# Performance work log

Measured on AMD Instinct MI355X. Metric: run time of the kernel, lower is better.

Reference implementation:

```python
import jax, jax.numpy as jnp
import numpy as np

NB_SITES = 16
K = 32            # nb_intervals
H = 512           # hidden_dim
EMB = 8           # embedding_dim
OUT = 3 * K + 3   # widths K + heights K + derivs K+1 + center_x + center_y
D = EMB * (NB_SITES - 1)
MIN_BIN = 1e-3
MIN_DER = 1e-3
B = 4096


def invsymlu(x):
    # inverse symmetric linear unit: x+1 for x>=0, 1/(1-x) for x<0
    return jnp.where(x >= 0, x + 1.0, 1.0 / (1.0 - x))


def freq_embed(x):
    # (...,) -> (..., EMB): 4 sin + 4 cos frequencies
    div = jnp.exp(jnp.arange(0, EMB, 2, dtype=jnp.float32) * (-jnp.log(100.0) / EMB))
    xe = x[..., None] * div
    return jnp.concatenate([jnp.sin(xe), jnp.cos(xe)], axis=-1)


def layernorm(x, s, b, eps=1e-6):
    m = jnp.mean(x, axis=-1, keepdims=True)
    v = jnp.var(x, axis=-1, keepdims=True)
    return (x - m) * jax.lax.rsqrt(v + eps) * s + b


def rqs_forward(inputs, uw, uh, ud, cx, cy):
    # inputs: (B,S); uw/uh: (B,S,K); ud: (B,S,K+1); cx/cy: (B,S)
    widths = MIN_BIN + invsymlu(uw)
    heights = MIN_BIN + invsymlu(uh)
    derivatives = MIN_DER + invsymlu(ud)

    pad = [(0, 0)] * (widths.ndim - 1) + [(1, 0)]
    cumwidths = jnp.pad(jnp.cumsum(widths, axis=-1), pad)
    cumwidths = cumwidths - cumwidths[..., -1:] / 2 + cx[..., None]
    cumheights = jnp.pad(jnp.cumsum(heights, axis=-1), pad)
    cumheights = cumheights - cumheights[..., -1:] / 2 + cy[..., None]

    left = inputs < cumwidths[..., 0]
    right = inputs >= cumwidths[..., -1]
    outputs = jnp.where(left, cumheights[..., 0] - (cumwidths[..., 0] - inputs) * derivatives[..., 0], 0.0)
    outputs = jnp.where(right, (inputs - cumwidths[..., -1]) * derivatives[..., -1] + cumheights[..., -1], outputs)
    logabsdet = jnp.where(left, jnp.log(derivatives[..., 0]), 0.0)
    logabsdet = jnp.where(right, jnp.log(derivatives[..., -1]), logabsdet)
    inside = ~(left | right)

    xs = jnp.where(inside, inputs, cx)
    # searchsorted via broadcast compare over K+1 knots
    bin_idx = (jnp.sum((xs[..., None] >= cumwidths), axis=-1) - 1)[..., None]

    take = lambda a: jnp.take_along_axis(a, bin_idx, axis=-1)[..., 0]
    icw = take(cumwidths)
    ibw = take(widths)
    ich = take(cumheights)
    delta = heights / widths
    idl = take(delta)
    ider = take(derivatives)
    iderp = take(derivatives[..., 1:])
    ih = take(heights)

    theta = (xs - icw) / ibw
    tomt = theta * (1 - theta)
    num = ih * (idl * theta ** 2 + ider * tomt)
    den = idl + (ider + iderp - 2 * idl) * tomt
    outputs = jnp.where(inside, ich + num / den, outputs)
    dnum = idl ** 2 * (iderp * theta ** 2 + 2 * idl * tomt + ider * (1 - theta) ** 2)
    logabsdet = jnp.where(inside, jnp.log(dnum) - 2 * jnp.log(den), logabsdet)
    return outputs, logabsdet


def setup_inputs() -> dict:
    ks = jax.random.split(jax.random.key(0), 8)
    S1 = NB_SITES - 1
    x = jax.random.normal(ks[0], (B, NB_SITES), jnp.float32)
    bias0 = jax.random.normal(ks[1], (OUT,), jnp.float32) * 0.1
    W0 = jax.random.normal(ks[2], (S1, D, H), jnp.float32) * (2.0 / D) ** 0.5
    W1 = jax.random.normal(ks[3], (S1, H, H), jnp.float32) * (2.0 / H) ** 0.5
    W2 = jax.random.normal(ks[4], (S1, H, H), jnp.float32) * (2.0 / H) ** 0.5
    Wf = jax.random.normal(ks[5], (S1, H, OUT), jnp.float32) * (2.0 / H) ** 0.5
    zH = jnp.zeros((S1, H), jnp.float32)
    oH = jnp.ones((S1, H), jnp.float32)
    return dict(x=x, bias0=bias0,
                W0=W0, b0=zH, ln0s=oH, ln0b=zH,
                W1=W1, b1=zH, ln1s=oH, ln1b=zH,
                W2=W2, b2=zH, ln2s=oH, ln2b=zH,
                Wf=Wf, bf=jnp.zeros((S1, OUT), jnp.float32))


def reference(x, bias0, W0, b0, ln0s, ln0b, W1, b1, ln1s, ln1b, W2, b2, ln2s, ln2b, Wf, bf):
    Bn = x.shape[0]
    S1 = NB_SITES - 1
    # embeddings of sites 0..S-2, flattened site-major: (B, D)
    e = freq_embed(x[:, :S1]).reshape(Bn, D)
    # causal per-site mask: site s (1..S-1) sees first EMB*s features
    site = jnp.arange(1, NB_SITES)
    mask = (jnp.arange(D)[None, :] < EMB * site[:, None]).astype(x.dtype)  # (S-1, D)
    Wm = W0 * mask[:, :, None]

    h = jnp.einsum('bd,sdh->bsh', e, Wm) + b0
    h = layernorm(jax.nn.gelu(h), ln0s, ln0b)
    y = jnp.einsum('bsh,shk->bsk', h, W1) + b1 + h   # residual
    y = layernorm(jax.nn.gelu(y), ln1s, ln1b)
    z = jnp.einsum('bsh,shk->bsk', y, W2) + b2 + y   # residual
    z = layernorm(jax.nn.gelu(z), ln2s, ln2b)
    p = jnp.einsum('bsh,sho->bso', z, Wf) + bf        # (B, S-1, OUT)

    p0 = jnp.broadcast_to(bias0, (Bn, 1, OUT))        # site 0: BiasOnlyNet
    params = jnp.concatenate([p0, p], axis=1)         # (B, S, OUT)

    uw = params[..., :K]
    uh = params[..., K:2 * K]
    ud = params[..., 2 * K:3 * K + 1]
    cx = params[..., 3 * K + 1]
    cy = params[..., 3 * K + 2]
    out, lad = rqs_forward(x, uw, uh, ud, cx, cy)
    return out, lad.sum(-1)
```

## Files before the change

kernel.cpp:

```cpp
#include <hip/hip_runtime.h>
#include <hip/hip_bf16.h>
#include <cstdint>
#include <cstddef>

typedef _Float16 f16;
typedef __attribute__((ext_vector_type(8))) _Float16 f16x8;
typedef __attribute__((ext_vector_type(4))) float f32x4;

#define DI __device__ __forceinline__

constexpr int BATCH  = 4096;
constexpr int S1     = 15;
constexpr int DPAD   = 128;
constexpr int H      = 512;
constexpr int OUTC   = 99;
constexpr int OUTPAD = 112;

DI float gelu_tanh(float x) {
  float t = 1.5957691216057308f * (x + 0.044715f * x * x * x);
  return x / (1.f + __expf(-t));
}

DI void gload16(const void* g, void* l) {
  __builtin_amdgcn_global_load_lds(
      (const __attribute__((address_space(1))) void*)g,
      (__attribute__((address_space(3))) void*)l, 16, 0, 0);
}

__global__ void embed_kernel(const float* __restrict__ x, f16* __restrict__ e) {
  const int b = blockIdx.x, d = threadIdx.x;
  float v = 0.f;
  if (d < 120) {
    const float divs[4] = {1.f, 0.31622776601683794f, 0.1f, 0.03162277660168379f};
    int site = d >> 3, j = d & 7;
    float arg = x[b * 16 + site] * divs[j & 3];
    v = (j < 4) ? sinf(arg) : cosf(arg);
  }
  e[b * DPAD + d] = (f16)v;
}

__global__ __launch_bounds__(256) void transpose_conv_kernel(
    const float* __restrict__ src, f16* __restrict__ dsth, f16* __restrict__ dstl,
    int K, int N, int Kpad, int Npad, int maskMul) {
  __shared__ float tile[32][33];
  const int s  = blockIdx.z;
  const int kb = blockIdx.x * 32, nb = blockIdx.y * 32;
  const int tx = threadIdx.x & 31, ty = threadIdx.x >> 5;
  for (int i = ty; i < 32; i += 8) {
    int k = kb + i, n = nb + tx;
    tile[i][tx] = (k < K && n < N) ? src[((size_t)s * K + k) * N + n] : 0.f;
  }
  __syncthreads();
  const int klim = maskMul ? maskMul * (s + 1) : 0x7FFFFFFF;
  for (int i = ty; i < 32; i += 8) {
    int n = nb + i, k = kb + tx;
    if (n < Npad && k < Kpad) {
      float v = (k < klim) ? tile[tx][i] : 0.f;
      size_t o = ((size_t)s * Npad + n) * Kpad + k;
      f16 h = (f16)v;
      dsth[o] = h;
      dstl[o] = (f16)(v - (float)h);
    }
  }
}

template<bool RES>
__global__ __launch_bounds__(512) void gemm_ln_kernel(
    const f16* __restrict__ A, const f16* __restrict__ Wh, const f16* __restrict__ Wl,
    const float* __restrict__ bias, const float* __restrict__ lns,
    const float* __restrict__ lnb, f16* __restrict__ out,
    int M, int Kd, int strideAS) {
  constexpr int BM = 64, BN = 512, BK = 64;
  constexpr int WM = 32, WN = 128, FM = 2, FN = 8;
  extern __shared__ f16 smem[];
  f16* const Aev = smem;
  f16* const Aod = smem + BM * BK;
  f16* const B0  = smem + 2 * BM * BK;
  f16* const B1  = B0 + BN * BK;

  const int n    = gridDim.x;
  const int b    = blockIdx.x;
  const int w    = (b & 7) * (n >> 3) + (b >> 3);
  const int srel = w >> 6;
  const int m0   = (w & 63) * BM;

  const f16* ap  = A  + (size_t)srel * strideAS + (size_t)m0 * Kd;
  const f16* wph = Wh + (size_t)srel * BN * Kd;
  const f16* wpl = Wl + (size_t)srel * BN * Kd;
  const int tid = threadIdx.x, wbase = tid & ~63;
  const int wave = tid >> 6, lane = tid & 63;
  const int wr = wave >> 2, wc = wave & 3;
  const int laneRow = lane & 15;
  const int hi      = lane >> 4;

  const int rA  = tid >> 3;
  const int cg8 = (((tid & 7) ^ (rA & 7)) << 3);
  const uint32_t offA = (uint32_t)rA * (uint32_t)Kd + cg8;
  uint32_t offB[8];
#pragma unroll
  for (int j = 0; j < 8; ++j)
    offB[j] = (uint32_t)(j * 64 + rA) * (uint32_t)Kd + cg8;

  auto stageB = [&](const f16* __restrict__ gbase, uint32_t koff, f16* lds) {
#pragma unroll
    for (int j = 0; j < 8; ++j)
      gload16(gbase + offB[j] + koff, lds + ((j * 512 + wbase) << 3));
  };
  auto stageA = [&](uint32_t koff, f16* lds) {
    gload16(ap + offA + koff, lds + (wbase << 3));
  };

  f32x4 acc[FM][FN] = {};
  auto mma = [&](const f16* __restrict__ Ab, const f16* __restrict__ Bb) {
#pragma unroll
    for (int kk = 0; kk < BK / 32; ++kk) {
      const int cc = kk * 4 + hi;
      f16x8 a[FM];
#pragma unroll
      for (int mi = 0; mi < FM; ++mi) {
        const int row = wr * WM + mi * 16 + laneRow;
        a[mi] = *reinterpret_cast<const f16x8*>(&Ab[row * BK + ((cc ^ (row & 7)) << 3)]);
      }
#pragma unroll
      for (int ni = 0; ni < FN; ++ni) {
        const int row = wc * WN + ni * 16 + laneRow;
        f16x8 bv = *reinterpret_cast<const f16x8*>(&Bb[row * BK + ((cc ^ (row & 7)) << 3)]);
#pragma unroll
        for (int mi = 0; mi < FM; ++mi)
          acc[mi][ni] = __builtin_amdgcn_mfma_f32_16x16x32_f16(a[mi], bv, acc[mi][ni], 0, 0, 0);
      }
    }
  };

  stageA(0, Aev);
  stageB(wph, 0, B0);
  const int NT = Kd / BK;
  for (int t = 0; t < NT; t += 2) {
    __syncthreads();
    stageB(wpl, (uint32_t)t * BK, B1);
    mma(Aev, B0);
    __syncthreads();
    stageA((uint32_t)(t + 1) * BK, Aod);
    stageB(wph, (uint32_t)(t + 1) * BK, B0);
    mma(Aev, B1);
    __syncthreads();
    stageB(wpl, (uint32_t)(t + 1) * BK, B1);
    mma(Aod, B0);
    __syncthreads();
    if (t + 2 < NT) {
      stageA((uint32_t)(t + 2) * BK, Aev);
      stageB(wph, (uint32_t)(t + 2) * BK, B0);
    }
    mma(Aod, B1);
  }

  const int rbase = hi * 4;
  float bv[FN], sv[FN], bb[FN];
#pragma unroll
  for (int ni = 0; ni < FN; ++ni) {
    const int gn = wc * WN + ni * 16 + laneRow;
    bv[ni] = bias[srel * H + gn];
    sv[ni] = lns[srel * H + gn];
    bb[ni] = lnb[srel * H + gn];
  }
  float lsum[FM][4], lsq[FM][4];
#pragma unroll
  for (int mi = 0; mi < FM; ++mi)
#pragma unroll
    for (int r = 0; r < 4; ++r) { lsum[mi][r] = 0.f; lsq[mi][r] = 0.f; }
#pragma unroll
  for (int mi = 0; mi < FM; ++mi)
#pragma unroll
    for (int r = 0; r < 4; ++r) {
      const int row = wr * WM + mi * 16 + rbase + r;
#pragma unroll
      for (int ni = 0; ni < FN; ++ni) {
        const int gn = wc * WN + ni * 16 + laneRow;
        float y = acc[mi][ni][r] + bv[ni];
        if constexpr (RES)
          y += (float)A[(size_t)srel * strideAS + (size_t)(m0 + row) * Kd + gn];
        float g = gelu_tanh(y);
        acc[mi][ni][r] = g;
        lsum[mi][r] += g;
        lsq[mi][r]  += g * g;
      }
    }
#pragma unroll
  for (int o = 1; o < 16; o <<= 1)
#pragma unroll
    for (int mi = 0; mi < FM; ++mi)
#pragma unroll
      for (int r = 0; r < 4; ++r) {
        lsum[mi][r] += __shfl_xor(lsum[mi][r], o, 64);
        lsq[mi][r]  += __shfl_xor(lsq[mi][r], o, 64);
      }
  __syncthreads();
  float* red = reinterpret_cast<float*>(smem);
  if (laneRow == 0) {
#pragma unroll
    for (int mi = 0; mi < FM; ++mi)
#pragma unroll
      for (int r = 0; r < 4; ++r) {
        const int row = wr * WM + mi * 16 + rbase + r;
        red[(row * 4 + wc) * 2 + 0] = lsum[mi][r];
        red[(row * 4 + wc) * 2 + 1] = lsq[mi][r];
      }
  }
  __syncthreads();
#pragma unroll
  for (int mi = 0; mi < FM; ++mi)
#pragma unroll
    for (int r = 0; r < 4; ++r) {
      const int row = wr * WM + mi * 16 + rbase + r;
      float sum = 0.f, sq = 0.f;
#pragma unroll
      for (int w4 = 0; w4 < 4; ++w4) {
        sum += red[(row * 4 + w4) * 2 + 0];
        sq  += red[(row * 4 + w4) * 2 + 1];
      }
      const float mean = sum * (1.f / 512.f);
      const float var  = sq * (1.f / 512.f) - mean * mean;
      const float rstd = 1.f / sqrtf(var + 1e-6f);
#pragma unroll
      for (int ni = 0; ni < FN; ++ni) {
        const int gn = wc * WN + ni * 16 + laneRow;
        float z = (acc[mi][ni][r] - mean) * rstd * sv[ni] + bb[ni];
        out[((size_t)srel * M + m0 + row) * H + gn] = (f16)z;
      }
    }
}

__global__ __launch_bounds__(512) void gemm_out_kernel(
    const f16* __restrict__ A, const f16* __restrict__ Wh, const f16* __restrict__ Wl,
    const float* __restrict__ bias, float* __restrict__ out,
    int M, int Kd, int strideAS) {
  constexpr int BM = 128, BN = 112, BK = 64;
  constexpr int CPR = BK / 8, SWZ = CPR - 1;
  constexpr int FN = 7;
  extern __shared__ f16 smem[];
  f16* As  = smem;
  f16* Bhs = As + BM * BK;
  f16* Bls = Bhs + BN * BK;

  const int s  = blockIdx.z;
  const int m0 = blockIdx.x * BM;
  const f16* ap  = A  + (size_t)s * strideAS + (size_t)m0 * Kd;
  const f16* wph = Wh + (size_t)s * BN * Kd;
  const f16* wpl = Wl + (size_t)s * BN * Kd;
  const int tid = threadIdx.x, wbase = tid & ~63;
  const int wave = tid >> 6, lane = tid & 63;
  const int wr = wave;
  f32x4 acc[FN] = {};
  const int laneRow = lane & 15;
  const int hi      = lane >> 4;

  for (int k0 = 0; k0 < Kd; k0 += BK) {
    __syncthreads();
#pragma unroll
    for (int base = 0; base < BM * CPR; base += 512) {
      const int idx = base + tid;
      const int r = idx / CPR, c = idx % CPR, cg = c ^ (r & SWZ);
      gload16(ap + (size_t)r * Kd + k0 + cg * 8, As + (size_t)(base + wbase) * 8);
    }
#pragma unroll
    for (int base = 0; base < BN * CPR; base += 512) {
      const int idx = base + tid;
      if (idx < BN * CPR) {
        const int r = idx / CPR, c = idx % CPR, cg = c ^ (r & SWZ);
        const size_t go = (size_t)r * Kd + k0 + cg * 8;
        gload16(wph + go, Bhs + (size_t)(base + wbase) * 8);
        gload16(wpl + go, Bls + (size_t)(base + wbase) * 8);
      }
    }
    __syncthreads();
#pragma unroll
    for (int kk = 0; kk < BK / 32; ++kk) {
      const int cc = kk * 4 + hi;
      const int rowA = wr * 16 + laneRow;
      f16x8 a = *reinterpret_cast<const f16x8*>(&As[rowA * BK + ((cc ^ (rowA & SWZ)) << 3)]);
#pragma unroll
      for (int ni = 0; ni < FN; ++ni) {
        const int row = ni * 16 + laneRow;
        const int off = row * BK + ((cc ^ (row & SWZ)) << 3);
        f16x8 bh = *reinterpret_cast<const f16x8*>(&Bhs[off]);
        f16x8 bl = *reinterpret_cast<const f16x8*>(&Bls[off]);
        acc[ni] = __builtin_amdgcn_mfma_f32_16x16x32_f16(a, bh, acc[ni], 0, 0, 0);
        acc[ni] = __builtin_amdgcn_mfma_f32_16x16x32_f16(a, bl, acc[ni], 0, 0, 0);
      }
    }
  }

  const int rbase = hi * 4;
#pragma unroll
  for (int ni = 0; ni < FN; ++ni)
#pragma unroll
    for (int r = 0; r < 4; ++r) {
      const int gm = m0 + wr * 16 + rbase + r;
      const int gn = ni * 16 + laneRow;
      if (gn < OUTC)
        out[((size_t)s * M + gm) * OUTC + gn] = acc[ni][r] + bias[s * OUTC + gn];
    }
}

DI float invsymlu(float u) { return u >= 0.f ? u + 1.f : 1.f / (1.f - u); }

__global__ __launch_bounds__(128) void spline_kernel(
    const float* __restrict__ x, const float* __restrict__ bias0,
    const float* __restrict__ p, float* __restrict__ out0, float* __restrict__ ladbuf) {
  __shared__ float prm[128 * 101];
  const int i  = blockIdx.x;
  const int b0 = blockIdx.y * 128;
  if (i == 0) {
    for (int idx = threadIdx.x; idx < 128 * OUTC; idx += 128)
      prm[(idx / OUTC) * 101 + idx % OUTC] = bias0[idx % OUTC];
  } else {
    const float* src = p + ((size_t)(i - 1) * BATCH + b0) * OUTC;
    for (int idx = threadIdx.x; idx < 128 * OUTC; idx += 128)
      prm[(idx / OUTC) * 101 + idx % OUTC] = src[idx];
  }
  __syncthreads();
  const float* P = &prm[threadIdx.x * 101];
  const int b = b0 + threadIdx.x;
  const float inp = x[b * 16 + i];

  float tw = 0.f, th = 0.f;
  for (int k = 0; k < 32; ++k) tw += 0.001f + invsymlu(P[k]);
  for (int k = 0; k < 32; ++k) th += 0.001f + invsymlu(P[32 + k]);
  const float cx = P[97], cy = P[98];
  const float w0 = cx - 0.5f * tw, wK = cx + 0.5f * tw;
  const float h0 = cy - 0.5f * th, hK = cy + 0.5f * th;
  const float d0 = 0.001f + invsymlu(P[64]);
  const float dK = 0.001f + invsymlu(P[96]);
  float outv, lad;
  if (inp < w0) {
    outv = h0 - (w0 - inp) * d0;
    lad  = logf(d0);
  } else if (inp >= wK) {
    outv = (inp - wK) * dK + hK;
    lad  = logf(dK);
  } else {
    float run = w0, icw = w0, ibw = 1.f;
    int bin = 0;
    for (int k = 0; k < 32; ++k) {
      float wk = 0.001f + invsymlu(P[k]);
      if (inp >= run) { bin = k; icw = run; ibw = wk; }
      run += wk;
    }
    float runh = h0;
    for (int k = 0; k < bin; ++k) runh += 0.001f + invsymlu(P[32 + k]);
    const float ih    = 0.001f + invsymlu(P[32 + bin]);
    const float ich   = runh;
    const float ider  = 0.001f + invsymlu(P[64 + bin]);
    const float iderp = 0.001f + invsymlu(P[64 + bin + 1]);
    const float idl   = ih / ibw;
    const float theta = (inp - icw) / ibw;
    const float omt   = 1.f - theta;
    const float tomt  = theta * omt;
    const float num   = ih * (idl * theta * theta + ider * tomt);
    const float den   = idl + (ider + iderp - 2.f * idl) * tomt;
    outv = ich + num / den;
    const float dnum = idl * idl * (iderp * theta * theta + 2.f * idl * tomt + ider * omt * omt);
    lad = logf(dnum) - 2.f * logf(den);
  }
  out0[b * 16 + i]   = outv;
  ladbuf[b * 16 + i] = lad;
}

__global__ void lad_reduce_kernel(const float* __restrict__ ladbuf, float* __restrict__ out1) {
  const int b = blockIdx.x * 256 + threadIdx.x;
  float s = 0.f;
#pragma unroll
  for (int i = 0; i < 16; ++i) s += ladbuf[b * 16 + i];
  out1[b] = s;
}

extern "C" void kernel_launch(void* const* d_in, const int* in_sizes, int n_in,
                              void* d_out, int out_size, void* d_ws, size_t ws_size,
                              hipStream_t stream) {
  const float* x     = (const float*)d_in[0];
  const float* bias0 = (const float*)d_in[1];
  const float* W0    = (const float*)d_in[2];
  const float* b0    = (const float*)d_in[3];
  const float* ln0s  = (const float*)d_in[4];
  const float* ln0b  = (const float*)d_in[5];
  const float* W1    = (const float*)d_in[6];
  const float* b1    = (const float*)d_in[7];
  const float* ln1s  = (const float*)d_in[8];
  const float* ln1b  = (const float*)d_in[9];
  const float* W2    = (const float*)d_in[10];
  const float* b2    = (const float*)d_in[11];
  const float* ln2s  = (const float*)d_in[12];
  const float* ln2b  = (const float*)d_in[13];
  const float* Wf    = (const float*)d_in[14];
  const float* bfb   = (const float*)d_in[15];
  float* out0 = (float*)d_out;
  float* out1 = out0 + BATCH * 16;

  const size_t fixedBytes =
      (size_t)BATCH * DPAD * 2 +
      2 * ((size_t)S1 * H * DPAD * 2) +
      4 * ((size_t)S1 * H * H * 2) +
      2 * ((size_t)S1 * OUTPAD * H * 2) +
      (size_t)S1 * BATCH * OUTC * 4 +
      (size_t)BATCH * 16 * 4 +
      64 * 256;
  const size_t perSiteP = 2 * ((size_t)BATCH * H * 2);
  int CH = 1;
  if (ws_size > fixedBytes) {
    size_t c = (ws_size - fixedBytes) / perSiteP;
    CH = (c >= (size_t)S1) ? S1 : (c < 1 ? 1 : (int)c);
  }
  const int nPasses = (S1 + CH - 1) / CH;
  const int baseSz  = S1 / nPasses;
  const int remSz   = S1 % nPasses;

  char* ws = (char*)d_ws;
  size_t off = 0;
  auto take = [&](size_t bytes) {
    char* q = ws + off;
    off += (bytes + 255) & ~(size_t)255;
    return q;
  };
  f16* e     = (f16*)take((size_t)BATCH * DPAD * 2);
  f16* W0Th  = (f16*)take((size_t)S1 * H * DPAD * 2);
  f16* W0Tl  = (f16*)take((size_t)S1 * H * DPAD * 2);
  f16* W1Th  = (f16*)take((size_t)S1 * H * H * 2);
  f16* W1Tl  = (f16*)take((size_t)S1 * H * H * 2);
  f16* W2Th  = (f16*)take((size_t)S1 * H * H * 2);
  f16* W2Tl  = (f16*)take((size_t)S1 * H * H * 2);
  f16* WfTh  = (f16*)take((size_t)S1 * OUTPAD * H * 2);
  f16* WfTl  = (f16*)take((size_t)S1 * OUTPAD * H * 2);
  f16* P1    = (f16*)take((size_t)CH * BATCH * H * 2);
  f16* P2    = (f16*)take((size_t)CH * BATCH * H * 2);
  float* pbuf = (float*)take((size_t)S1 * BATCH * OUTC * 4);
  float* ladb = (float*)take((size_t)BATCH * 16 * 4);

  embed_kernel<<<BATCH, 128, 0, stream>>>(x, e);
  transpose_conv_kernel<<<dim3(4, 16, S1), 256, 0, stream>>>(W0, W0Th, W0Tl, 120, H, DPAD, H, 8);
  transpose_conv_kernel<<<dim3(16, 16, S1), 256, 0, stream>>>(W1, W1Th, W1Tl, H, H, H, H, 0);
  transpose_conv_kernel<<<dim3(16, 16, S1), 256, 0, stream>>>(W2, W2Th, W2Tl, H, H, H, H, 0);
  transpose_conv_kernel<<<dim3(16, 4, S1), 256, 0, stream>>>(Wf, WfTh, WfTl, H, OUTC, H, OUTPAD, 0);

  const size_t ldsFused = (size_t)(2 * 64 + 2 * 512) * 64 * 2;
  const size_t ldsOut   = (size_t)(128 + 112 + 112) * 64 * 2;

  int sb = 0;
  for (int pass = 0; pass < nPasses; ++pass) {
    const int nz = baseSz + (pass < remSz ? 1 : 0);
    const int gridFused = (BATCH / 64) * nz;
    gemm_ln_kernel<false><<<gridFused, 512, ldsFused, stream>>>(
        e, W0Th + (size_t)sb * H * DPAD, W0Tl + (size_t)sb * H * DPAD,
        b0 + sb * H, ln0s + sb * H, ln0b + sb * H, P2, BATCH, DPAD, 0);
    gemm_ln_kernel<true><<<gridFused, 512, ldsFused, stream>>>(
        P2, W1Th + (size_t)sb * H * H, W1Tl + (size_t)sb * H * H,
        b1 + sb * H, ln1s + sb * H, ln1b + sb * H, P1, BATCH, H, BATCH * H);
    gemm_ln_kernel<true><<<gridFused, 512, ldsFused, stream>>>(
        P1, W2Th + (size_t)sb * H * H, W2Tl + (size_t)sb * H * H,
        b2 + sb * H, ln2s + sb * H, ln2b + sb * H, P2, BATCH, H, BATCH * H);
    gemm_out_kernel<<<dim3(BATCH / 128, 1, nz), 512, ldsOut, stream>>>(
        P2, WfTh + (size_t)sb * OUTPAD * H, WfTl + (size_t)sb * OUTPAD * H,
        bfb + sb * OUTC, pbuf + (size_t)sb * BATCH * OUTC, BATCH, H, BATCH * H);
    sb += nz;
  }

  spline_kernel<<<dim3(16, 32), 128, 0, stream>>>(x, bias0, pbuf, out0, ladb);
  lad_reduce_kernel<<<BATCH / 256, 256, 0, stream>>>(ladb, out1);
}
```

Baseline: 364.8 us.

## Unfuse GEMM from GELU+LayerNorm; retile GEMM to 256x128 with f32 intermediate

Splits the fused GEMM+GELU+LayerNorm kernel into a GEMM that writes pre-activation y (bias plus residual) to an f32 buffer and a separate row-wise GELU+LayerNorm kernel. The GEMM tile moves from 64x512 to 256x128, which raises A reuse and lowers the per-block weight traffic that the full-row tile needed for the in-kernel LayerNorm. The cost is an extra f32 round trip of the activations through memory, three extra launches per pass, and a larger workspace per site, which may shrink the chunk size.

```diff
diff --git a/kernel.cpp b/kernel.cpp
--- a/kernel.cpp
+++ b/kernel.cpp
@@ -65,13 +65,12 @@
 }
 
 template<bool RES>
-__global__ __launch_bounds__(512) void gemm_ln_kernel(
+__global__ __launch_bounds__(512) void gemm_y_kernel(
     const f16* __restrict__ A, const f16* __restrict__ Wh, const f16* __restrict__ Wl,
-    const float* __restrict__ bias, const float* __restrict__ lns,
-    const float* __restrict__ lnb, f16* __restrict__ out,
+    const float* __restrict__ bias, float* __restrict__ ybuf,
     int M, int Kd, int strideAS) {
-  constexpr int BM = 64, BN = 512, BK = 64;
-  constexpr int WM = 32, WN = 128, FM = 2, FN = 8;
+  constexpr int BM = 256, BN = 128, BK = 64;
+  constexpr int WM = 64, WN = 64, FM = 4, FN = 4;
   extern __shared__ f16 smem[];
   f16* const Aev = smem;
   f16* const Aod = smem + BM * BK;
@@ -82,32 +81,36 @@
   const int b    = blockIdx.x;
   const int w    = (b & 7) * (n >> 3) + (b >> 3);
   const int srel = w >> 6;
-  const int m0   = (w & 63) * BM;
+  const int rem  = w & 63;
+  const int m0   = (rem >> 2) * BM;
+  const int n0   = (rem & 3) * BN;
 
   const f16* ap  = A  + (size_t)srel * strideAS + (size_t)m0 * Kd;
-  const f16* wph = Wh + (size_t)srel * BN * Kd;
-  const f16* wpl = Wl + (size_t)srel * BN * Kd;
+  const f16* wph = Wh + ((size_t)srel * H + n0) * Kd;
+  const f16* wpl = Wl + ((size_t)srel * H + n0) * Kd;
   const int tid = threadIdx.x, wbase = tid & ~63;
   const int wave = tid >> 6, lane = tid & 63;
-  const int wr = wave >> 2, wc = wave & 3;
+  const int wr = wave >> 1, wc = wave & 1;
   const int laneRow = lane & 15;
   const int hi      = lane >> 4;
 
   const int rA  = tid >> 3;
   const int cg8 = (((tid & 7) ^ (rA & 7)) << 3);
-  const uint32_t offA = (uint32_t)rA * (uint32_t)Kd + cg8;
-  uint32_t offB[8];
-#pragma unroll
-  for (int j = 0; j < 8; ++j)
-    offB[j] = (uint32_t)(j * 64 + rA) * (uint32_t)Kd + cg8;
-
+  uint32_t offA[4], offB[2];
+#pragma unroll
+  for (int j = 0; j < 4; ++j) offA[j] = (uint32_t)(j * 64 + rA) * (uint32_t)Kd + cg8;
+#pragma unroll
+  for (int j = 0; j < 2; ++j) offB[j] = (uint32_t)(j * 64 + rA) * (uint32_t)Kd + cg8;
+
+  auto stageA = [&](uint32_t koff, f16* lds) {
+#pragma unroll
+    for (int j = 0; j < 4; ++j)
+      gload16(ap + offA[j] + koff, lds + ((j * 512 + wbase) << 3));
+  };
   auto stageB = [&](const f16* __restrict__ gbase, uint32_t koff, f16* lds) {
 #pragma unroll
-    for (int j = 0; j < 8; ++j)
+    for (int j = 0; j < 2; ++j)
       gload16(gbase + offB[j] + koff, lds + ((j * 512 + wbase) << 3));
-  };
-  auto stageA = [&](uint32_t koff, f16* lds) {
-    gload16(ap + offA + koff, lds + (wbase << 3));
   };
 
   f32x4 acc[FM][FN] = {};
@@ -154,80 +157,53 @@
     mma(Aod, B1);
   }
 
-  const int rbase = hi * 4;
-  float bv[FN], sv[FN], bb[FN];
 #pragma unroll
   for (int ni = 0; ni < FN; ++ni) {
-    const int gn = wc * WN + ni * 16 + laneRow;
-    bv[ni] = bias[srel * H + gn];
-    sv[ni] = lns[srel * H + gn];
-    bb[ni] = lnb[srel * H + gn];
-  }
-  float lsum[FM][4], lsq[FM][4];
-#pragma unroll
-  for (int mi = 0; mi < FM; ++mi)
-#pragma unroll
-    for (int r = 0; r < 4; ++r) { lsum[mi][r] = 0.f; lsq[mi][r] = 0.f; }
-#pragma unroll
-  for (int mi = 0; mi < FM; ++mi)
-#pragma unroll
-    for (int r = 0; r < 4; ++r) {
-      const int row = wr * WM + mi * 16 + rbase + r;
-#pragma unroll
-      for (int ni = 0; ni < FN; ++ni) {
-        const int gn = wc * WN + ni * 16 + laneRow;
-        float y = acc[mi][ni][r] + bv[ni];
+    const int colg = n0 + wc * WN + ni * 16 + laneRow;
+    const float bvv = bias[srel * H + colg];
+#pragma unroll
+    for (int mi = 0; mi < FM; ++mi)
+#pragma unroll
+      for (int r = 0; r < 4; ++r) {
+        const int row = wr * WM + mi * 16 + hi * 4 + r;
+        float y = acc[mi][ni][r] + bvv;
         if constexpr (RES)
-          y += (float)A[(size_t)srel * strideAS + (size_t)(m0 + row) * Kd + gn];
-        float g = gelu_tanh(y);
-        acc[mi][ni][r] = g;
-        lsum[mi][r] += g;
-        lsq[mi][r]  += g * g;
+          y += (float)A[(size_t)srel * strideAS + (size_t)(m0 + row) * Kd + colg];
+        ybuf[((size_t)srel * M + m0 + row) * H + colg] = y;
       }
-    }
-#pragma unroll
-  for (int o = 1; o < 16; o <<= 1)
-#pragma unroll
-    for (int mi = 0; mi < FM; ++mi)
-#pragma unroll
-      for (int r = 0; r < 4; ++r) {
-        lsum[mi][r] += __shfl_xor(lsum[mi][r], o, 64);
-        lsq[mi][r]  += __shfl_xor(lsq[mi][r], o, 64);
-      }
-  __syncthreads();
-  float* red = reinterpret_cast<float*>(smem);
-  if (laneRow == 0) {
-#pragma unroll
-    for (int mi = 0; mi < FM; ++mi)
-#pragma unroll
-      for (int r = 0; r < 4; ++r) {
-        const int row = wr * WM + mi * 16 + rbase + r;
-        red[(row * 4 + wc) * 2 + 0] = lsum[mi][r];
-        red[(row * 4 + wc) * 2 + 1] = lsq[mi][r];
-      }
-  }
-  __syncthreads();
-#pragma unroll
-  for (int mi = 0; mi < FM; ++mi)
-#pragma unroll
-    for (int r = 0; r < 4; ++r) {
-      const int row = wr * WM + mi * 16 + rbase + r;
-      float sum = 0.f, sq = 0.f;
-#pragma unroll
-      for (int w4 = 0; w4 < 4; ++w4) {
-        sum += red[(row * 4 + w4) * 2 + 0];
-        sq  += red[(row * 4 + w4) * 2 + 1];
-      }
-      const float mean = sum * (1.f / 512.f);
-      const float var  = sq * (1.f / 512.f) - mean * mean;
-      const float rstd = 1.f / sqrtf(var + 1e-6f);
-#pragma unroll
-      for (int ni = 0; ni < FN; ++ni) {
-        const int gn = wc * WN + ni * 16 + laneRow;
-        float z = (acc[mi][ni][r] - mean) * rstd * sv[ni] + bb[ni];
-        out[((size_t)srel * M + m0 + row) * H + gn] = (f16)z;
-      }
-    }
+  }
+}
+
+__global__ __launch_bounds__(256) void gelu_ln_f32_kernel(
+    const float* __restrict__ ybuf, f16* __restrict__ zbuf,
+    const float* __restrict__ lns, const float* __restrict__ lnb) {
+  const int row  = blockIdx.x * 4 + (threadIdx.x >> 6);
+  const int lane = threadIdx.x & 63;
+  const float* yp = ybuf + (size_t)row * H + lane * 8;
+  float4 v0 = *reinterpret_cast<const float4*>(yp);
+  float4 v1 = *reinterpret_cast<const float4*>(yp + 4);
+  float g[8];
+  g[0] = gelu_tanh(v0.x); g[1] = gelu_tanh(v0.y); g[2] = gelu_tanh(v0.z); g[3] = gelu_tanh(v0.w);
+  g[4] = gelu_tanh(v1.x); g[5] = gelu_tanh(v1.y); g[6] = gelu_tanh(v1.z); g[7] = gelu_tanh(v1.w);
+  float sum = 0.f, sq = 0.f;
+#pragma unroll
+  for (int j = 0; j < 8; ++j) { sum += g[j]; sq += g[j] * g[j]; }
+#pragma unroll
+  for (int o = 32; o > 0; o >>= 1) {
+    sum += __shfl_xor(sum, o, 64);
+    sq  += __shfl_xor(sq, o, 64);
+  }
+  const float mean = sum * (1.f / 512.f);
+  const float var  = sq * (1.f / 512.f) - mean * mean;
+  const float rstd = 1.f / sqrtf(var + 1e-6f);
+  const int site = row / BATCH;
+  const float* sp = lns + site * H + lane * 8;
+  const float* bp = lnb + site * H + lane * 8;
+  f16x8 outv;
+#pragma unroll
+  for (int j = 0; j < 8; ++j)
+    outv[j] = (f16)((g[j] - mean) * rstd * sp[j] + bp[j]);
+  *reinterpret_cast<f16x8*>(&zbuf[(size_t)row * H + lane * 8]) = outv;
 }
 
 __global__ __launch_bounds__(512) void gemm_out_kernel(
@@ -404,7 +380,7 @@
       (size_t)S1 * BATCH * OUTC * 4 +
       (size_t)BATCH * 16 * 4 +
       64 * 256;
-  const size_t perSiteP = 2 * ((size_t)BATCH * H * 2);
+  const size_t perSiteP = (size_t)BATCH * H * 4 + 2 * ((size_t)BATCH * H * 2);
   int CH = 1;
   if (ws_size > fixedBytes) {
     size_t c = (ws_size - fixedBytes) / perSiteP;
@@ -430,6 +406,7 @@
   f16* W2Tl  = (f16*)take((size_t)S1 * H * H * 2);
   f16* WfTh  = (f16*)take((size_t)S1 * OUTPAD * H * 2);
   f16* WfTl  = (f16*)take((size_t)S1 * OUTPAD * H * 2);
+  float* ybuf = (float*)take((size_t)CH * BATCH * H * 4);
   f16* P1    = (f16*)take((size_t)CH * BATCH * H * 2);
   f16* P2    = (f16*)take((size_t)CH * BATCH * H * 2);
   float* pbuf = (float*)take((size_t)S1 * BATCH * OUTC * 4);
@@ -441,22 +418,26 @@
   transpose_conv_kernel<<<dim3(16, 16, S1), 256, 0, stream>>>(W2, W2Th, W2Tl, H, H, H, H, 0);
   transpose_conv_kernel<<<dim3(16, 4, S1), 256, 0, stream>>>(Wf, WfTh, WfTl, H, OUTC, H, OUTPAD, 0);
 
-  const size_t ldsFused = (size_t)(2 * 64 + 2 * 512) * 64 * 2;
-  const size_t ldsOut   = (size_t)(128 + 112 + 112) * 64 * 2;
+  const size_t ldsGemm = (size_t)(2 * 256 + 2 * 128) * 64 * 2;
+  const size_t ldsOut  = (size_t)(128 + 112 + 112) * 64 * 2;
 
   int sb = 0;
   for (int pass = 0; pass < nPasses; ++pass) {
     const int nz = baseSz + (pass < remSz ? 1 : 0);
-    const int gridFused = (BATCH / 64) * nz;
-    gemm_ln_kernel<false><<<gridFused, 512, ldsFused, stream>>>(
+    const int gridG = 64 * nz;
+    const int gridL = nz * BATCH / 4;
+    gemm_y_kernel<false><<<gridG, 512, ldsGemm, stream>>>(
         e, W0Th + (size_t)sb * H * DPAD, W0Tl + (size_t)sb * H * DPAD,
-        b0 + sb * H, ln0s + sb * H, ln0b + sb * H, P2, BATCH, DPAD, 0);
-    gemm_ln_kernel<true><<<gridFused, 512, ldsFused, stream>>>(
+        b0 + sb * H, ybuf, BATCH, DPAD, 0);
+    gelu_ln_f32_kernel<<<gridL, 256, 0, stream>>>(ybuf, P2, ln0s + sb * H, ln0b + sb * H);
+    gemm_y_kernel<true><<<gridG, 512, ldsGemm, stream>>>(
         P2, W1Th + (size_t)sb * H * H, W1Tl + (size_t)sb * H * H,
-        b1 + sb * H, ln1s + sb * H, ln1b + sb * H, P1, BATCH, H, BATCH * H);
-    gemm_ln_kernel<true><<<gridFused, 512, ldsFused, stream>>>(
+        b1 + sb * H, ybuf, BATCH, H, BATCH * H);
+    gelu_ln_f32_kernel<<<gridL, 256, 0, stream>>>(ybuf, P1, ln1s + sb * H, ln1b + sb * H);
+    gemm_y_kernel<true><<<gridG, 512, ldsGemm, stream>>>(
         P1, W2Th + (size_t)sb * H * H, W2Tl + (size_t)sb * H * H,
-        b2 + sb * H, ln2s + sb * H, ln2b + sb * H, P2, BATCH, H, BATCH * H);
+        b2 + sb * H, ybuf, BATCH, H, BATCH * H);
+    gelu_ln_f32_kernel<<<gridL, 256, 0, stream>>>(ybuf, P2, ln2s + sb * H, ln2b + sb * H);
     gemm_out_kernel<<<dim3(BATCH / 128, 1, nz), 512, ldsOut, stream>>>(
         P2, WfTh + (size_t)sb * OUTPAD * H, WfTl + (size_t)sb * OUTPAD * H,
         bfb + sb * OUTC, pbuf + (size_t)sb * BATCH * OUTC, BATCH, H, BATCH * H);
```

Result: slower. 382.9 us (+4.9%).
